# Kernel optimization log

Hardware: AMD Instinct MI355X
Metric: run time of the kernel (lower is better)

The kernel has to match this reference:

```python
import jax, jax.numpy as jnp
import numpy as np
import math

B, S, D = 2, 2048, 2048
H, HK = 32, 8          # query heads, kv heads
HD = D // H            # 64
REP = H // HK          # 4


def setup_inputs() -> dict:
    key = jax.random.key(0)
    ks = jax.random.split(key, 6)
    x = jax.random.normal(ks[0], (B, S, D), jnp.float32)
    # RoPE tables, rotate_half convention: halves duplicated along last dim
    inv_freq = 1.0 / (10000.0 ** (jnp.arange(0, HD, 2, dtype=jnp.float32) / HD))
    freqs = jnp.arange(S, dtype=jnp.float32)[:, None] * inv_freq[None, :]  # [S, HD/2]
    cos = jnp.concatenate([jnp.cos(freqs), jnp.cos(freqs)], axis=-1)       # [S, HD]
    sin = jnp.concatenate([jnp.sin(freqs), jnp.sin(freqs)], axis=-1)
    attn_mask = jnp.tril(jnp.ones((S, S), dtype=bool))
    std = 1.0 / math.sqrt(D)
    wq = jax.random.normal(ks[1], (D, D), jnp.float32) * std
    wk = jax.random.normal(ks[2], (HK * HD, D), jnp.float32) * std
    wv = jax.random.normal(ks[3], (HK * HD, D), jnp.float32) * std
    wo = jax.random.normal(ks[4], (D, D), jnp.float32) * std
    return {"x": x, "cos": cos, "sin": sin, "attn_mask": attn_mask,
            "wq": wq, "wk": wk, "wv": wv, "wo": wo}


def _rotate_half(t):
    h = t.shape[-1] // 2
    return jnp.concatenate([-t[..., h:], t[..., :h]], axis=-1)


def reference(x, cos, sin, attn_mask, wq, wk, wv, wo):
    b, s, d = x.shape
    q = (x @ wq.T).reshape(b, s, H, HD).transpose(0, 2, 1, 3)    # [b,H,s,hd]
    k = (x @ wk.T).reshape(b, s, HK, HD).transpose(0, 2, 1, 3)   # [b,HK,s,hd]
    v = (x @ wv.T).reshape(b, s, HK, HD).transpose(0, 2, 1, 3)
    c = cos[:s][None, None]
    sn = sin[:s][None, None]
    q = q * c + _rotate_half(q) * sn
    k = k * c + _rotate_half(k) * sn
    # GQA: group query heads instead of repeat_interleave'ing KV
    # repeat_interleave order == reshape (HK, REP): heads [g*REP : (g+1)*REP] share kv group g
    qg = q.reshape(b, HK, REP, s, HD)
    scores = jnp.einsum('bgrsd,bgtd->bgrst', qg, k) / math.sqrt(HD)  # [b,HK,REP,s,s]
    m = attn_mask[None, None, None, :, :]
    scores = jnp.where(m, scores, -jnp.inf)
    attn = jax.nn.softmax(scores, axis=-1)
    out = jnp.einsum('bgrst,bgtd->bgrsd', attn, v)                  # [b,HK,REP,s,hd]
    out = out.reshape(b, H, s, HD).transpose(0, 2, 1, 3).reshape(b, s, d)
    return out @ wo.T
```

## Files before the change

### kernel.cpp

```cpp
#include <hip/hip_runtime.h>
#include <hip/hip_bf16.h>
#include <math.h>

typedef __hip_bfloat16 bf16;
typedef __attribute__((ext_vector_type(8))) short bf16x8;
typedef __attribute__((ext_vector_type(4))) short short4v;
typedef __attribute__((ext_vector_type(4))) float f32x4;

static constexpr int B = 2, S = 2048, D = 2048, H = 32, HK = 8, HD = 64;
static constexpr int M = B * S;
static constexpr int NKV = HK * HD;
static constexpr int QKV3 = D + 2 * NKV;
static constexpr float SCALE2 = 0.125f * 1.44269504f;

__device__ __forceinline__ short bfbits(float x) {
  bf16 h = __float2bfloat16(x);
  return *reinterpret_cast<short*>(&h);
}

__device__ __forceinline__ float bf2f(short bits) {
  unsigned int u = ((unsigned int)(unsigned short)bits) << 16;
  return __builtin_bit_cast(float, u);
}

__device__ __forceinline__ void gl_lds16(const bf16* gp, bf16* lp) {
  __builtin_amdgcn_global_load_lds(
      (const __attribute__((address_space(1))) unsigned int*)(const void*)gp,
      (__attribute__((address_space(3))) unsigned int*)(void*)lp, 16, 0, 0);
}

struct alignas(8) bf4 { bf16 v[4]; };
static constexpr int N4_X  = M * D / 4;
static constexpr int N4_WQ = D * D / 4;
static constexpr int N4_WK = NKV * D / 4;
static constexpr int E0 = N4_X;
static constexpr int E1 = E0 + N4_WQ;
static constexpr int E2 = E1 + N4_WK;
static constexpr int E3 = E2 + N4_WK;
static constexpr int E4 = E3 + N4_WQ;
__global__ __launch_bounds__(256) void cast_all_kernel(const float* __restrict__ x,
                                                       const float* __restrict__ wq,
                                                       const float* __restrict__ wk,
                                                       const float* __restrict__ wv,
                                                       const float* __restrict__ wo,
                                                       bf16* __restrict__ xb,
                                                       bf16* __restrict__ wqkv,
                                                       bf16* __restrict__ wob) {
  int i = blockIdx.x * 256 + threadIdx.x;
  int stride = gridDim.x * 256;
  for (; i < E4; i += stride) {
    const float* s; bf16* d; int j;
    if (i < E0)      { s = x;  d = xb;   j = i; }
    else if (i < E1) { s = wq; d = wqkv; j = i - E0; }
    else if (i < E2) { s = wk; d = wqkv + (size_t)N4_WQ * 4; j = i - E1; }
    else if (i < E3) { s = wv; d = wqkv + (size_t)(N4_WQ + N4_WK) * 4; j = i - E2; }
    else             { s = wo; d = wob;  j = i - E3; }
    float4 f = reinterpret_cast<const float4*>(s)[j];
    bf4 o;
    o.v[0] = __float2bfloat16(f.x);
    o.v[1] = __float2bfloat16(f.y);
    o.v[2] = __float2bfloat16(f.z);
    o.v[3] = __float2bfloat16(f.w);
    reinterpret_cast<bf4*>(d)[j] = o;
  }
}

template <bool OUT_F32>
__global__ __launch_bounds__(256) void gemm_bt_kernel(const bf16* __restrict__ A,
                                                      const bf16* __restrict__ Bt,
                                                      void* __restrict__ C,
                                                      int Ndim, int Kdim) {
  __shared__ __align__(16) bf16 As[128][64];
  __shared__ __align__(16) bf16 Bs[128][64];
  const int tid = threadIdx.x;
  const int lane = tid & 63;
  const int w = tid >> 6;
  const int wm = w >> 1, wn = w & 1;
  const int r16 = lane & 15, g = lane >> 4;
  const int bm = blockIdx.y, bn = blockIdx.x;
  f32x4 acc[4][4] = {};

  const int nk = Kdim >> 6;
  for (int kt = 0; kt < nk; ++kt) {
    __syncthreads();
#pragma unroll
    for (int i = 0; i < 4; ++i) {
      int u = tid + i * 256;
      int rr = u >> 3, c8 = u & 7;
      int c8s = c8 ^ (rr & 7);
      gl_lds16(&A[(size_t)(bm * 128 + rr) * Kdim + kt * 64 + c8s * 8], &As[0][0] + (size_t)u * 8);
      gl_lds16(&Bt[(size_t)(bn * 128 + rr) * Kdim + kt * 64 + c8s * 8], &Bs[0][0] + (size_t)u * 8);
    }
    __syncthreads();
#pragma unroll
    for (int kc = 0; kc < 2; ++kc) {
      bf16x8 af[4], bfr[4];
      const int kq = kc * 4 + g;
#pragma unroll
      for (int m = 0; m < 4; ++m) {
        int ra = wm * 64 + m * 16 + r16;
        af[m] = *reinterpret_cast<const bf16x8*>(&As[ra][(kq ^ (ra & 7)) * 8]);
        int rb = wn * 64 + m * 16 + r16;
        bfr[m] = *reinterpret_cast<const bf16x8*>(&Bs[rb][(kq ^ (rb & 7)) * 8]);
      }
#pragma unroll
      for (int m = 0; m < 4; ++m)
#pragma unroll
        for (int n = 0; n < 4; ++n)
          acc[m][n] = __builtin_amdgcn_mfma_f32_16x16x32_bf16(af[m], bfr[n], acc[m][n], 0, 0, 0);
    }
  }
  const int row0 = bm * 128 + wm * 64 + g * 4;
  const int col0 = bn * 128 + wn * 64 + r16;
#pragma unroll
  for (int m = 0; m < 4; ++m)
#pragma unroll
    for (int n = 0; n < 4; ++n)
#pragma unroll
      for (int j = 0; j < 4; ++j) {
        size_t idx = (size_t)(row0 + m * 16 + j) * Ndim + col0 + n * 16;
        if (OUT_F32)
          reinterpret_cast<float*>(C)[idx] = acc[m][n][j];
        else
          reinterpret_cast<bf16*>(C)[idx] = __float2bfloat16(acc[m][n][j]);
      }
}

__global__ __launch_bounds__(256) void rope_k_kernel(bf16* __restrict__ t,
                                                     const float* __restrict__ cosb,
                                                     const float* __restrict__ sinb) {
  int idx = blockIdx.x * 256 + threadIdx.x;
  int i = idx & 31;
  int rest = idx >> 5;
  int hh = rest & 7;
  int s = (rest >> 3) % S;
  int b = rest / (8 * S);
  size_t base = ((size_t)b * S + s) * QKV3 + D + hh * HD;
  float x0 = __bfloat162float(t[base + i]);
  float x1 = __bfloat162float(t[base + i + 32]);
  float c = cosb[s * HD + i];
  float sn = sinb[s * HD + i];
  t[base + i] = __float2bfloat16(x0 * c - x1 * sn);
  t[base + i + 32] = __float2bfloat16(x1 * c + x0 * sn);
}

__global__ __launch_bounds__(256) void transpose_v_kernel(const bf16* __restrict__ qkv,
                                                          bf16* __restrict__ vt) {
  __shared__ bf16 tile[64][65];
  const int st = blockIdx.x;
  const int bk = blockIdx.y;
  const int b = bk >> 3, hk = bk & 7;
  const int tid = threadIdx.x;
#pragma unroll
  for (int i = 0; i < 16; ++i) {
    int idx = tid + i * 256;
    int rs = idx >> 6, c = idx & 63;
    tile[rs][c] = qkv[((size_t)b * S + st * 64 + rs) * QKV3 + (D + NKV) + hk * HD + c];
  }
  __syncthreads();
#pragma unroll
  for (int i = 0; i < 16; ++i) {
    int idx = tid + i * 256;
    int rh = idx >> 6, cs = idx & 63;
    int blk = cs >> 5, kvl = cs & 31;
    int pos = ((kvl >> 2) & 3) * 8 + ((kvl >> 4) << 2) + (kvl & 3);
    vt[(((size_t)b * HK + hk) * HD + rh) * S + st * 64 + blk * 32 + pos] = tile[cs][rh];
  }
}

__global__ __launch_bounds__(256, 2) void attn_kernel(const bf16* __restrict__ qkv,
                                                      const bf16* __restrict__ vt,
                                                      const float* __restrict__ cosb,
                                                      const float* __restrict__ sinb,
                                                      bf16* __restrict__ ao) {
  __shared__ __align__(16) bf16 Ksh[4][64 * 64];
  __shared__ __align__(16) bf16 Vsh[4][64 * 64];
  const int u = blockIdx.x;
  const int y = blockIdx.y;
  const int b = y >> 3, hk = y & 7;
  const int tid = threadIdx.x;
  const int w = tid >> 6;
  const int h = hk * 4 + w;
  const int lane = tid & 63;
  const int r = lane & 15, g = lane >> 4;

  const bf16* qp  = qkv + ((size_t)b * S) * QKV3 + h * HD;
  const bf16* kvp = qkv + ((size_t)b * S) * QKV3 + D + hk * HD;
  const bf16* vtp = vt + (((size_t)b * HK + hk) * HD) * S;
  const int srow = tid >> 3;
  const int sc8 = tid & 7;

  bf16x8 ones;
#pragma unroll
  for (int j = 0; j < 8; ++j) ones[j] = (short)0x3F80;

  auto stage64 = [&](int tl, int kv0) {
#pragma unroll
    for (int i = 0; i < 2; ++i) {
      int rr = srow + i * 32;
      int cs = sc8 ^ (rr & 7);
      gl_lds16(&kvp[(size_t)(kv0 + rr) * QKV3 + cs * 8], &Ksh[tl][((size_t)rr * 8 + sc8) * 8]);
    }
#pragma unroll
    for (int i = 0; i < 2; ++i) {
      int rr = srow + i * 32;
      int cs = sc8 ^ (rr & 7);
      gl_lds16(&vtp[(size_t)rr * S + kv0 + cs * 8], &Vsh[tl][((size_t)rr * 8 + sc8) * 8]);
    }
  };

  for (int pass = 0; pass < 2; ++pass) {
    const int qb = pass ? (2016 - u * 32) : (u * 32);
    bf16x8 qfr[2][2];
#pragma unroll
    for (int qq = 0; qq < 2; ++qq) {
      const int srowq = qb + qq * 16 + r;
      bf16x8 f0 = *reinterpret_cast<const bf16x8*>(&qp[(size_t)srowq * QKV3 + g * 8]);
      bf16x8 f1 = *reinterpret_cast<const bf16x8*>(&qp[(size_t)srowq * QKV3 + 32 + g * 8]);
      float4 c0 = reinterpret_cast<const float4*>(&cosb[(size_t)srowq * HD + g * 8])[0];
      float4 c1 = reinterpret_cast<const float4*>(&cosb[(size_t)srowq * HD + g * 8])[1];
      float4 s0 = reinterpret_cast<const float4*>(&sinb[(size_t)srowq * HD + g * 8])[0];
      float4 s1 = reinterpret_cast<const float4*>(&sinb[(size_t)srowq * HD + g * 8])[1];
      float cc[8] = {c0.x, c0.y, c0.z, c0.w, c1.x, c1.y, c1.z, c1.w};
      float ss[8] = {s0.x, s0.y, s0.z, s0.w, s1.x, s1.y, s1.z, s1.w};
#pragma unroll
      for (int j = 0; j < 8; ++j) {
        float x0 = bf2f(f0[j]), x1 = bf2f(f1[j]);
        qfr[qq][0][j] = bfbits((x0 * cc[j] - x1 * ss[j]) * SCALE2);
        qfr[qq][1][j] = bfbits((x1 * cc[j] + x0 * ss[j]) * SCALE2);
      }
    }

    f32x4 o[4][2] = {};
    f32x4 ol[2] = {};
    const int kv_end = qb + 32;
    const int nch = (kv_end + 127) >> 7;

    stage64(0, 0);
    stage64(1, 64);
    __syncthreads();
    for (int c = 0; c < nch; ++c) {
      const int base_t = (c & 1) * 2;
      if (c + 1 < nch) {
        const int nb = ((c + 1) & 1) * 2;
        stage64(nb, (c + 1) * 128);
        stage64(nb + 1, (c + 1) * 128 + 64);
      }
#pragma unroll
      for (int t = 0; t < 2; ++t) {
        const int kv0 = c * 128 + t * 64;
        if (kv0 >= kv_end) break;
        const int tl = base_t + t;
        const bool lasth = (kv0 + 64 >= kv_end);
        f32x4 scv[4][2] = {};
        __builtin_amdgcn_s_setprio(1);
#pragma unroll
        for (int f = 0; f < 4; ++f) {
          const int row = f * 16 + r;
#pragma unroll
          for (int hc = 0; hc < 2; ++hc) {
            bf16x8 kf = *reinterpret_cast<const bf16x8*>(
                &Ksh[tl][(size_t)row * 64 + (((hc * 4 + g) ^ (r & 7)) * 8)]);
            scv[f][0] = __builtin_amdgcn_mfma_f32_16x16x32_bf16(kf, qfr[0][hc], scv[f][0], 0, 0, 0);
            scv[f][1] = __builtin_amdgcn_mfma_f32_16x16x32_bf16(kf, qfr[1][hc], scv[f][1], 0, 0, 0);
          }
        }
        __builtin_amdgcn_s_setprio(0);
        if (lasth) {
#pragma unroll
          for (int qq = 0; qq < 2; ++qq) {
            const int qi = qb + qq * 16 + r;
#pragma unroll
            for (int f = 0; f < 4; ++f)
#pragma unroll
              for (int j = 0; j < 4; ++j)
                if (kv0 + f * 16 + g * 4 + j > qi) scv[f][qq][j] = -1e30f;
          }
        }
#pragma unroll
        for (int blk = 0; blk < 2; ++blk) {
          bf16x8 pb0, pb1;
#pragma unroll
          for (int jj = 0; jj < 8; ++jj) {
            const int f = blk * 2 + (jj >> 2), j = jj & 3;
            pb0[jj] = bfbits(exp2f(scv[f][0][j]));
            pb1[jj] = bfbits(exp2f(scv[f][1][j]));
          }
          __builtin_amdgcn_s_setprio(1);
          ol[0] = __builtin_amdgcn_mfma_f32_16x16x32_bf16(ones, pb0, ol[0], 0, 0, 0);
          ol[1] = __builtin_amdgcn_mfma_f32_16x16x32_bf16(ones, pb1, ol[1], 0, 0, 0);
#pragma unroll
          for (int d = 0; d < 4; ++d) {
            bf16x8 vf = *reinterpret_cast<const bf16x8*>(
                &Vsh[tl][(size_t)(d * 16 + r) * 64 + (((blk * 4 + g) ^ (r & 7)) * 8)]);
            o[d][0] = __builtin_amdgcn_mfma_f32_16x16x32_bf16(vf, pb0, o[d][0], 0, 0, 0);
            o[d][1] = __builtin_amdgcn_mfma_f32_16x16x32_bf16(vf, pb1, o[d][1], 0, 0, 0);
          }
          __builtin_amdgcn_s_setprio(0);
        }
      }
      __syncthreads();
    }
#pragma unroll
    for (int qq = 0; qq < 2; ++qq) {
      float inv = 1.0f / ol[qq][0];
#pragma unroll
      for (int d = 0; d < 4; ++d) {
        short4v ov;
        ov[0] = bfbits(o[d][qq][0] * inv);
        ov[1] = bfbits(o[d][qq][1] * inv);
        ov[2] = bfbits(o[d][qq][2] * inv);
        ov[3] = bfbits(o[d][qq][3] * inv);
        *reinterpret_cast<short4v*>(
            &ao[(((size_t)b * S + qb + qq * 16 + r) * H + h) * HD + d * 16 + g * 4]) = ov;
      }
    }
  }
}

extern "C" void kernel_launch(void* const* d_in, const int* in_sizes, int n_in,
                              void* d_out, int out_size, void* d_ws, size_t ws_size,
                              hipStream_t stream) {
  (void)in_sizes; (void)n_in; (void)out_size; (void)ws_size;
  const float* x    = (const float*)d_in[0];
  const float* cosb = (const float*)d_in[1];
  const float* sinb = (const float*)d_in[2];
  const float* wq   = (const float*)d_in[4];
  const float* wk   = (const float*)d_in[5];
  const float* wv   = (const float*)d_in[6];
  const float* wo   = (const float*)d_in[7];

  char* ws = (char*)d_ws;
  size_t off = 0;
  auto alloc = [&](size_t elems) {
    bf16* p = (bf16*)(ws + off);
    off = (off + elems * sizeof(bf16) + 255) & ~(size_t)255;
    return p;
  };
  bf16* xb    = alloc((size_t)M * D);
  bf16* wqkvb = alloc((size_t)QKV3 * D);
  bf16* wob   = alloc((size_t)D * D);
  bf16* qkvb  = alloc((size_t)M * QKV3);
  bf16* vtb   = alloc((size_t)B * HK * HD * S);
  bf16* aob   = alloc((size_t)M * D);

  cast_all_kernel<<<dim3(2048), dim3(256), 0, stream>>>(x, wq, wk, wv, wo, xb, wqkvb, wob);

  gemm_bt_kernel<false><<<dim3(QKV3 / 128, M / 128), 256, 0, stream>>>(xb, wqkvb, qkvb, QKV3, D);

  rope_k_kernel<<<dim3(B * S * 8 * 32 / 256), 256, 0, stream>>>(qkvb, cosb, sinb);

  transpose_v_kernel<<<dim3(S / 64, B * HK), 256, 0, stream>>>(qkvb, vtb);

  attn_kernel<<<dim3(32, B * HK), 256, 0, stream>>>(qkvb, vtb, cosb, sinb, aob);

  gemm_bt_kernel<true><<<dim3(D / 128, M / 128), 256, 0, stream>>>(aob, wob, d_out, D, D);
}
```

Measured before the change: 190.3 us.

## Split attention blocks to one query tile each with smaller LDS double buffer

Replaces the two-pass paired query-block scheme with one query tile per block, doubling the grid and ordering heavy tiles first. KV staging drops from 128-row to 64-row double-buffered chunks, halving LDS so launch bounds allow four blocks per CU. The aim is higher occupancy and better latency hiding. It gives up the explicit causal load pairing and adds more barriers per KV row.

```diff
diff --git a/kernel.cpp b/kernel.cpp
--- a/kernel.cpp
+++ b/kernel.cpp
@@ -168,13 +168,13 @@
   }
 }
 
-__global__ __launch_bounds__(256, 2) void attn_kernel(const bf16* __restrict__ qkv,
+__global__ __launch_bounds__(256, 4) void attn_kernel(const bf16* __restrict__ qkv,
                                                       const bf16* __restrict__ vt,
                                                       const float* __restrict__ cosb,
                                                       const float* __restrict__ sinb,
                                                       bf16* __restrict__ ao) {
-  __shared__ __align__(16) bf16 Ksh[4][64 * 64];
-  __shared__ __align__(16) bf16 Vsh[4][64 * 64];
+  __shared__ __align__(16) bf16 Ksh[2][64 * 64];
+  __shared__ __align__(16) bf16 Vsh[2][64 * 64];
   const int u = blockIdx.x;
   const int y = blockIdx.y;
   const int b = y >> 3, hk = y & 7;
@@ -194,126 +194,114 @@
 #pragma unroll
   for (int j = 0; j < 8; ++j) ones[j] = (short)0x3F80;
 
-  auto stage64 = [&](int tl, int kv0) {
+  auto stage64 = [&](int buf, int kv0) {
 #pragma unroll
     for (int i = 0; i < 2; ++i) {
       int rr = srow + i * 32;
       int cs = sc8 ^ (rr & 7);
-      gl_lds16(&kvp[(size_t)(kv0 + rr) * QKV3 + cs * 8], &Ksh[tl][((size_t)rr * 8 + sc8) * 8]);
+      gl_lds16(&kvp[(size_t)(kv0 + rr) * QKV3 + cs * 8], &Ksh[buf][((size_t)rr * 8 + sc8) * 8]);
     }
 #pragma unroll
     for (int i = 0; i < 2; ++i) {
       int rr = srow + i * 32;
       int cs = sc8 ^ (rr & 7);
-      gl_lds16(&vtp[(size_t)rr * S + kv0 + cs * 8], &Vsh[tl][((size_t)rr * 8 + sc8) * 8]);
+      gl_lds16(&vtp[(size_t)rr * S + kv0 + cs * 8], &Vsh[buf][((size_t)rr * 8 + sc8) * 8]);
     }
   };
 
-  for (int pass = 0; pass < 2; ++pass) {
-    const int qb = pass ? (2016 - u * 32) : (u * 32);
-    bf16x8 qfr[2][2];
-#pragma unroll
-    for (int qq = 0; qq < 2; ++qq) {
-      const int srowq = qb + qq * 16 + r;
-      bf16x8 f0 = *reinterpret_cast<const bf16x8*>(&qp[(size_t)srowq * QKV3 + g * 8]);
-      bf16x8 f1 = *reinterpret_cast<const bf16x8*>(&qp[(size_t)srowq * QKV3 + 32 + g * 8]);
-      float4 c0 = reinterpret_cast<const float4*>(&cosb[(size_t)srowq * HD + g * 8])[0];
-      float4 c1 = reinterpret_cast<const float4*>(&cosb[(size_t)srowq * HD + g * 8])[1];
-      float4 s0 = reinterpret_cast<const float4*>(&sinb[(size_t)srowq * HD + g * 8])[0];
-      float4 s1 = reinterpret_cast<const float4*>(&sinb[(size_t)srowq * HD + g * 8])[1];
-      float cc[8] = {c0.x, c0.y, c0.z, c0.w, c1.x, c1.y, c1.z, c1.w};
-      float ss[8] = {s0.x, s0.y, s0.z, s0.w, s1.x, s1.y, s1.z, s1.w};
-#pragma unroll
-      for (int j = 0; j < 8; ++j) {
-        float x0 = bf2f(f0[j]), x1 = bf2f(f1[j]);
-        qfr[qq][0][j] = bfbits((x0 * cc[j] - x1 * ss[j]) * SCALE2);
-        qfr[qq][1][j] = bfbits((x1 * cc[j] + x0 * ss[j]) * SCALE2);
-      }
-    }
-
-    f32x4 o[4][2] = {};
-    f32x4 ol[2] = {};
-    const int kv_end = qb + 32;
-    const int nch = (kv_end + 127) >> 7;
-
-    stage64(0, 0);
-    stage64(1, 64);
+  const int qb = 2016 - u * 32;
+  bf16x8 qfr[2][2];
+#pragma unroll
+  for (int qq = 0; qq < 2; ++qq) {
+    const int srowq = qb + qq * 16 + r;
+    bf16x8 f0 = *reinterpret_cast<const bf16x8*>(&qp[(size_t)srowq * QKV3 + g * 8]);
+    bf16x8 f1 = *reinterpret_cast<const bf16x8*>(&qp[(size_t)srowq * QKV3 + 32 + g * 8]);
+    float4 c0 = reinterpret_cast<const float4*>(&cosb[(size_t)srowq * HD + g * 8])[0];
+    float4 c1 = reinterpret_cast<const float4*>(&cosb[(size_t)srowq * HD + g * 8])[1];
+    float4 s0 = reinterpret_cast<const float4*>(&sinb[(size_t)srowq * HD + g * 8])[0];
+    float4 s1 = reinterpret_cast<const float4*>(&sinb[(size_t)srowq * HD + g * 8])[1];
+    float cc[8] = {c0.x, c0.y, c0.z, c0.w, c1.x, c1.y, c1.z, c1.w};
+    float ss[8] = {s0.x, s0.y, s0.z, s0.w, s1.x, s1.y, s1.z, s1.w};
+#pragma unroll
+    for (int j = 0; j < 8; ++j) {
+      float x0 = bf2f(f0[j]), x1 = bf2f(f1[j]);
+      qfr[qq][0][j] = bfbits((x0 * cc[j] - x1 * ss[j]) * SCALE2);
+      qfr[qq][1][j] = bfbits((x1 * cc[j] + x0 * ss[j]) * SCALE2);
+    }
+  }
+
+  f32x4 o[4][2] = {};
+  f32x4 ol[2] = {};
+  const int kv_end = qb + 32;
+  const int nch = (kv_end + 63) >> 6;
+
+  stage64(0, 0);
+  __syncthreads();
+  for (int c = 0; c < nch; ++c) {
+    const int cur = c & 1;
+    const int kv0 = c * 64;
+    const bool lastc = (c == nch - 1);
+    if (!lastc) stage64(cur ^ 1, kv0 + 64);
+    f32x4 scv[4][2] = {};
+    __builtin_amdgcn_s_setprio(1);
+#pragma unroll
+    for (int f = 0; f < 4; ++f) {
+      const int row = f * 16 + r;
+#pragma unroll
+      for (int hc = 0; hc < 2; ++hc) {
+        bf16x8 kf = *reinterpret_cast<const bf16x8*>(
+            &Ksh[cur][(size_t)row * 64 + (((hc * 4 + g) ^ (r & 7)) * 8)]);
+        scv[f][0] = __builtin_amdgcn_mfma_f32_16x16x32_bf16(kf, qfr[0][hc], scv[f][0], 0, 0, 0);
+        scv[f][1] = __builtin_amdgcn_mfma_f32_16x16x32_bf16(kf, qfr[1][hc], scv[f][1], 0, 0, 0);
+      }
+    }
+    __builtin_amdgcn_s_setprio(0);
+    if (lastc) {
+#pragma unroll
+      for (int qq = 0; qq < 2; ++qq) {
+        const int qi = qb + qq * 16 + r;
+#pragma unroll
+        for (int f = 0; f < 4; ++f)
+#pragma unroll
+          for (int j = 0; j < 4; ++j)
+            if (kv0 + f * 16 + g * 4 + j > qi) scv[f][qq][j] = -1e30f;
+      }
+    }
+#pragma unroll
+    for (int blk = 0; blk < 2; ++blk) {
+      bf16x8 pb0, pb1;
+#pragma unroll
+      for (int jj = 0; jj < 8; ++jj) {
+        const int f = blk * 2 + (jj >> 2), j = jj & 3;
+        pb0[jj] = bfbits(exp2f(scv[f][0][j]));
+        pb1[jj] = bfbits(exp2f(scv[f][1][j]));
+      }
+      __builtin_amdgcn_s_setprio(1);
+      ol[0] = __builtin_amdgcn_mfma_f32_16x16x32_bf16(ones, pb0, ol[0], 0, 0, 0);
+      ol[1] = __builtin_amdgcn_mfma_f32_16x16x32_bf16(ones, pb1, ol[1], 0, 0, 0);
+#pragma unroll
+      for (int d = 0; d < 4; ++d) {
+        bf16x8 vf = *reinterpret_cast<const bf16x8*>(
+            &Vsh[cur][(size_t)(d * 16 + r) * 64 + (((blk * 4 + g) ^ (r & 7)) * 8)]);
+        o[d][0] = __builtin_amdgcn_mfma_f32_16x16x32_bf16(vf, pb0, o[d][0], 0, 0, 0);
+        o[d][1] = __builtin_amdgcn_mfma_f32_16x16x32_bf16(vf, pb1, o[d][1], 0, 0, 0);
+      }
+      __builtin_amdgcn_s_setprio(0);
+    }
     __syncthreads();
-    for (int c = 0; c < nch; ++c) {
-      const int base_t = (c & 1) * 2;
-      if (c + 1 < nch) {
-        const int nb = ((c + 1) & 1) * 2;
-        stage64(nb, (c + 1) * 128);
-        stage64(nb + 1, (c + 1) * 128 + 64);
-      }
-#pragma unroll
-      for (int t = 0; t < 2; ++t) {
-        const int kv0 = c * 128 + t * 64;
-        if (kv0 >= kv_end) break;
-        const int tl = base_t + t;
-        const bool lasth = (kv0 + 64 >= kv_end);
-        f32x4 scv[4][2] = {};
-        __builtin_amdgcn_s_setprio(1);
-#pragma unroll
-        for (int f = 0; f < 4; ++f) {
-          const int row = f * 16 + r;
-#pragma unroll
-          for (int hc = 0; hc < 2; ++hc) {
-            bf16x8 kf = *reinterpret_cast<const bf16x8*>(
-                &Ksh[tl][(size_t)row * 64 + (((hc * 4 + g) ^ (r & 7)) * 8)]);
-            scv[f][0] = __builtin_amdgcn_mfma_f32_16x16x32_bf16(kf, qfr[0][hc], scv[f][0], 0, 0, 0);
-            scv[f][1] = __builtin_amdgcn_mfma_f32_16x16x32_bf16(kf, qfr[1][hc], scv[f][1], 0, 0, 0);
-          }
-        }
-        __builtin_amdgcn_s_setprio(0);
-        if (lasth) {
-#pragma unroll
-          for (int qq = 0; qq < 2; ++qq) {
-            const int qi = qb + qq * 16 + r;
-#pragma unroll
-            for (int f = 0; f < 4; ++f)
-#pragma unroll
-              for (int j = 0; j < 4; ++j)
-                if (kv0 + f * 16 + g * 4 + j > qi) scv[f][qq][j] = -1e30f;
-          }
-        }
-#pragma unroll
-        for (int blk = 0; blk < 2; ++blk) {
-          bf16x8 pb0, pb1;
-#pragma unroll
-          for (int jj = 0; jj < 8; ++jj) {
-            const int f = blk * 2 + (jj >> 2), j = jj & 3;
-            pb0[jj] = bfbits(exp2f(scv[f][0][j]));
-            pb1[jj] = bfbits(exp2f(scv[f][1][j]));
-          }
-          __builtin_amdgcn_s_setprio(1);
-          ol[0] = __builtin_amdgcn_mfma_f32_16x16x32_bf16(ones, pb0, ol[0], 0, 0, 0);
-          ol[1] = __builtin_amdgcn_mfma_f32_16x16x32_bf16(ones, pb1, ol[1], 0, 0, 0);
-#pragma unroll
-          for (int d = 0; d < 4; ++d) {
-            bf16x8 vf = *reinterpret_cast<const bf16x8*>(
-                &Vsh[tl][(size_t)(d * 16 + r) * 64 + (((blk * 4 + g) ^ (r & 7)) * 8)]);
-            o[d][0] = __builtin_amdgcn_mfma_f32_16x16x32_bf16(vf, pb0, o[d][0], 0, 0, 0);
-            o[d][1] = __builtin_amdgcn_mfma_f32_16x16x32_bf16(vf, pb1, o[d][1], 0, 0, 0);
-          }
-          __builtin_amdgcn_s_setprio(0);
-        }
-      }
-      __syncthreads();
-    }
-#pragma unroll
-    for (int qq = 0; qq < 2; ++qq) {
-      float inv = 1.0f / ol[qq][0];
-#pragma unroll
-      for (int d = 0; d < 4; ++d) {
-        short4v ov;
-        ov[0] = bfbits(o[d][qq][0] * inv);
-        ov[1] = bfbits(o[d][qq][1] * inv);
-        ov[2] = bfbits(o[d][qq][2] * inv);
-        ov[3] = bfbits(o[d][qq][3] * inv);
-        *reinterpret_cast<short4v*>(
-            &ao[(((size_t)b * S + qb + qq * 16 + r) * H + h) * HD + d * 16 + g * 4]) = ov;
-      }
+  }
+#pragma unroll
+  for (int qq = 0; qq < 2; ++qq) {
+    float inv = 1.0f / ol[qq][0];
+#pragma unroll
+    for (int d = 0; d < 4; ++d) {
+      short4v ov;
+      ov[0] = bfbits(o[d][qq][0] * inv);
+      ov[1] = bfbits(o[d][qq][1] * inv);
+      ov[2] = bfbits(o[d][qq][2] * inv);
+      ov[3] = bfbits(o[d][qq][3] * inv);
+      *reinterpret_cast<short4v*>(
+          &ao[(((size_t)b * S + qb + qq * 16 + r) * H + h) * HD + d * 16 + g * 4]) = ov;
     }
   }
 }
@@ -352,7 +340,7 @@
 
   transpose_v_kernel<<<dim3(S / 64, B * HK), 256, 0, stream>>>(qkvb, vtb);
 
-  attn_kernel<<<dim3(32, B * HK), 256, 0, stream>>>(qkvb, vtb, cosb, sinb, aob);
+  attn_kernel<<<dim3(64, B * HK), 256, 0, stream>>>(qkvb, vtb, cosb, sinb, aob);
 
   gemm_bt_kernel<true><<<dim3(D / 128, M / 128), 256, 0, stream>>>(aob, wob, d_out, D, D);
 }
```

Measured after the change: 221.3 us. +16.3%, slower.
